# Optimization experiments

Hardware: AMD Instinct MI355X
Metric: run time of the kernel (lower is better)

Reference implementation:

```python
import jax, jax.numpy as jnp
import numpy as np
from jax import lax

I, H, L, O = 5, 64, 3, 1  # input_size, hidden_size, num_layers, output_size
B, T = 1024, 256


def setup_inputs() -> dict:
    key = jax.random.key(0)
    ks = jax.random.split(key, 1 + 4 * L + 2)
    inp = {"x": jax.random.normal(ks[0], (B, T, I), dtype=jnp.float32)}
    s = 1.0 / np.sqrt(H)  # PyTorch LSTM init scale
    kidx = 1
    for l in range(L):
        in_dim = I if l == 0 else H
        inp[f"w_ih{l}"] = jax.random.uniform(ks[kidx], (4 * H, in_dim), minval=-s, maxval=s); kidx += 1
        inp[f"w_hh{l}"] = jax.random.uniform(ks[kidx], (4 * H, H), minval=-s, maxval=s); kidx += 1
        inp[f"b_ih{l}"] = jax.random.uniform(ks[kidx], (4 * H,), minval=-s, maxval=s); kidx += 1
        inp[f"b_hh{l}"] = jax.random.uniform(ks[kidx], (4 * H,), minval=-s, maxval=s); kidx += 1
    inp["w_fc"] = jax.random.uniform(ks[kidx], (O, H), minval=-s, maxval=s); kidx += 1
    inp["b_fc"] = jax.random.uniform(ks[kidx], (O,), minval=-s, maxval=s)
    return inp


def _lstm_layer(x, w_ih, w_hh, b_ih, b_hh):
    # x: [B, T, in_dim] -> hidden sequence [B, T, H]
    b, t = x.shape[0], x.shape[1]
    h0 = jnp.zeros((b, H), dtype=x.dtype)
    c0 = jnp.zeros((b, H), dtype=x.dtype)
    # precompute input contribution for all timesteps (one big GEMM)
    xg = jnp.einsum('bti,gi->btg', x, w_ih) + (b_ih + b_hh)  # [B, T, 4H]

    def step(carry, xg_t):
        h, c = carry
        gates = xg_t + h @ w_hh.T  # [B, 4H], PyTorch gate order: i, f, g, o
        i, f, g, o = jnp.split(gates, 4, axis=-1)
        i = jax.nn.sigmoid(i)
        f = jax.nn.sigmoid(f)
        g = jnp.tanh(g)
        o = jax.nn.sigmoid(o)
        c = f * c + i * g
        h = o * jnp.tanh(c)
        return (h, c), h

    _, hs = lax.scan(step, (h0, c0), jnp.swapaxes(xg, 0, 1))  # hs: [T, B, H]
    return jnp.swapaxes(hs, 0, 1)


def reference(x, w_ih0, w_hh0, b_ih0, b_hh0, w_ih1, w_hh1, b_ih1, b_hh1,
              w_ih2, w_hh2, b_ih2, b_hh2, w_fc, b_fc):
    out = _lstm_layer(x, w_ih0, w_hh0, b_ih0, b_hh0)
    out = _lstm_layer(out, w_ih1, w_hh1, b_ih1, b_hh1)
    out = _lstm_layer(out, w_ih2, w_hh2, b_ih2, b_hh2)
    # dropout is identity in eval mode
    return out[:, -1, :] @ w_fc.T + b_fc  # [B, O]
```

## Files before the change

kernel.cpp:

```cpp
#include <hip/hip_runtime.h>
#include <math.h>


typedef __attribute__((ext_vector_type(8))) short bf16x8;
typedef __attribute__((ext_vector_type(4))) float f32x4;

constexpr int Hh  = 64;
constexpr int Tt  = 256;
constexpr int In  = 5;
constexpr int TBr = 4;
constexpr int NB  = 256;
constexpr int NT  = 768;

constexpr int RB_ = 144;
constexpr int LB  = 2304;
constexpr int PB  = 8192;

__device__ __forceinline__ float tanhc(float x) {
    return fmaf(2.0f, __builtin_amdgcn_rcpf(1.0f + __expf(-2.0f * x)), -1.0f);
}

__device__ __forceinline__ short f2bf_rne(float f) {
    union { float f; unsigned u; } v; v.f = f;
    unsigned r = (v.u + 0x7fffu + ((v.u >> 16) & 1u)) >> 16;
    return (short)r;
}
__device__ __forceinline__ void split_bf(float f, short& hi, short& lo) {
    union { float f; unsigned u; } v; v.f = f;
    hi = (short)(v.u >> 16);
    union { unsigned u; float f; } h; h.u = v.u & 0xffff0000u;
    float r = f - h.f;
    union { float f; unsigned u; } w; w.f = r;
    lo = (short)(w.u >> 16);
}

__device__ __forceinline__ bf16x8 ldwfrag(const float* __restrict__ W,
                                          int n, int stride, int k0, int kmax) {
    bf16x8 r;
    #pragma unroll
    for (int j = 0; j < 8; ++j) {
        int k = k0 + j;
        float f = (k < kmax) ? W[n * stride + k] : 0.0f;
        r[j] = f2bf_rne(f);
    }
    return r;
}

#define MF(A, B, C) __builtin_amdgcn_mfma_f32_16x16x32_bf16(A, B, C, 0, 0, 0)

#define LBAR() asm volatile("s_waitcnt lgkmcnt(0)\n\ts_barrier" ::: "memory")

#define STEP(TI, RO, RBp, WR) do {                                           \
    const int ti_ = (TI);                                                    \
    const bool act_ = (wg == 0) ? (ti_ < Tt)                                 \
                    : (wg == 1) ? (ti_ >= 1 && ti_ <= Tt)                    \
                                : (ti_ >= 2);                                \
    if (act_) {                                                              \
        if (xmask) {                   \
            _Pragma("unroll")                                                \
            for (int jj = 0; jj < In; ++jj) {                                \
                short h_, l_; split_bf(xr[jj], h_, l_);                      \
                xhi[jj] = h_; xlo[jj] = l_;                                  \
            }                                                                \
        }                                                                    \
        if (lreal) {             \
            oh0 = *(const bf16x8*)(RO);                                      \
            oh1 = *(const bf16x8*)((RO) + 64);                               \
            if (wg > 0) {                                                    \
                bh0 = *(const bf16x8*)(RBp);                                 \
                bh1 = *(const bf16x8*)((RBp) + 64);                          \
            }                                                                \
        }                                                                    \
        f32x4 acc[4];                                                        \
        __builtin_amdgcn_s_setprio(1);                                       \
        _Pragma("unroll")                                                    \
        for (int gi = 0; gi < 4; ++gi)                                       \
            acc[gi] = MF(oh0, WH[gi][0], bsv[gi]);            \
        _Pragma("unroll")                                                    \
        for (int gi = 0; gi < 4; ++gi)                                       \
            acc[gi] = MF(oh1, WH[gi][1], acc[gi]);                           \
        if (wg == 0) {                               \
            _Pragma("unroll")                                                \
            for (int gi = 0; gi < 4; ++gi)                                   \
                acc[gi] = MF(xhi, WI[gi][0], acc[gi]);                       \
            _Pragma("unroll")                                                \
            for (int gi = 0; gi < 4; ++gi)                                   \
                acc[gi] = MF(xlo, WI[gi][0], acc[gi]);                       \
        } else {                             \
            _Pragma("unroll")                                                \
            for (int gi = 0; gi < 4; ++gi)                                   \
                acc[gi] = MF(bh0, WI[gi][0], acc[gi]);                       \
            _Pragma("unroll")                                                \
            for (int gi = 0; gi < 4; ++gi)                                   \
                acc[gi] = MF(bh1, WI[gi][1], acc[gi]);                       \
        }                                                                    \
        __builtin_amdgcn_s_setprio(0);                                       \
        if (xmask && ti_ + 1 < Tt) {                    \
            _Pragma("unroll")                                                \
            for (int jj = 0; jj < In; ++jj)                                  \
                xr[jj] = x[xbase + (size_t)(ti_ + 1) * In + jj];             \
        }                                                                    \
          \
        float ei = __expf(-acc[0][0]);                                       \
        float ef = __expf(-acc[1][0]);                                       \
        float eg = __expf(-2.0f * acc[2][0]);                                \
        float eo = __expf(-acc[3][0]);                                       \
        float ig = (1.0f - eg) *                                             \
                   __builtin_amdgcn_rcpf((1.0f + ei) * (1.0f + eg));         \
        float fv = __builtin_amdgcn_rcpf(1.0f + ef);                         \
        float cn = fmaf(fv, c0, ig);                                         \
        c0 = cn;                                                             \
        float ov = __builtin_amdgcn_rcpf(1.0f + eo);                         \
        float hn = ov * tanhc(cn);                                           \
        unsigned pk_;                                                        \
        asm("v_cvt_pk_bf16_f32 %0, %1, %2" : "=v"(pk_) : "v"(hn), "v"(hn));  \
        *(short*)(WR) = (short)pk_;                                          \
        if (wg == 2) h2f[kg][ub + col] = hn;        \
    }                                                                        \
    LBAR();                                                                  \
} while (0)

__global__ __launch_bounds__(NT, 2) void lstm3_mfma(
    const float* __restrict__ x,
    const float* __restrict__ w_ih0, const float* __restrict__ w_hh0,
    const float* __restrict__ b_ih0, const float* __restrict__ b_hh0,
    const float* __restrict__ w_ih1, const float* __restrict__ w_hh1,
    const float* __restrict__ b_ih1, const float* __restrict__ b_hh1,
    const float* __restrict__ w_ih2, const float* __restrict__ w_hh2,
    const float* __restrict__ b_ih2, const float* __restrict__ b_hh2,
    const float* __restrict__ w_fc,  const float* __restrict__ b_fc,
    float* __restrict__ out)
{
    __shared__ short hb[2][PB / 2];
    __shared__ float h2f[TBr][Hh];

    const int tid = threadIdx.x;
    const int l   = tid & 63;
    const int wid = tid >> 6;
    const int wg  = wid >> 2;
    const int w4  = wid & 3;
    const int ub  = w4 * 16;
    const int col = l & 15;
    const int kg  = l >> 4;
    const int b0  = blockIdx.x * TBr;
    const bool lreal = ((col & 3) == 0);

    for (int i = tid; i < PB * 2 / 4; i += NT) ((int*)hb)[i] = 0;

    const float* whh = (wg == 0) ? w_hh0 : (wg == 1) ? w_hh1 : w_hh2;
    const float* wih = (wg == 0) ? w_ih0 : (wg == 1) ? w_ih1 : w_ih2;
    const float* bih = (wg == 0) ? b_ih0 : (wg == 1) ? b_ih1 : b_ih2;
    const float* bhh = (wg == 0) ? b_hh0 : (wg == 1) ? b_hh1 : b_hh2;

    bf16x8 WH[4][2], WI[4][2];
    f32x4  bsv[4];
    #pragma unroll
    for (int gi = 0; gi < 4; ++gi) {
        int n = gi * 64 + ub + col;
        float bs_ = bih[n] + bhh[n];
        bsv[gi] = (f32x4){bs_, bs_, bs_, bs_};
        #pragma unroll
        for (int kt = 0; kt < 2; ++kt) {
            WH[gi][kt] = ldwfrag(whh, n, Hh, kt * 32 + kg * 8, Hh);
            if (wg == 0) {
                WI[gi][kt] = (kt == 0) ? ldwfrag(wih, n, In, kg * 8, In)
                                       : ldwfrag(wih, n, In, 64, 0);
            } else {
                WI[gi][kt] = ldwfrag(wih, n, Hh, kt * 32 + kg * 8, Hh);
            }
        }
    }

    char* hbB = (char*)hb;
    const int lbelow = (wg > 0) ? (wg - 1) : 0;
    const int lown   = (wg > 0) ? LB : 0;
    const char* rbB_ = hbB + lbelow * LB + col * RB_ + kg * 16;
    const char* rbA_ = rbB_ + PB;
    const char* roA  = rbA_ + lown;
    const char* roB  = rbB_ + lown;
    char* wrA = hbB + wg * LB + (kg * 4) * RB_ + (ub + col) * 2;
    char* wrB = wrA + PB;

    const bool xmask = (wg == 0) && (kg == 0) && lreal;
    const size_t xbase = (size_t)(b0 + (col >> 2)) * Tt * In;
    float xr[5] = {0.f, 0.f, 0.f, 0.f, 0.f};
    bf16x8 xhi, xlo, oh0, oh1, bh0, bh1;
    #pragma unroll
    for (int j = 0; j < 8; ++j) {
        xhi[j] = 0; xlo[j] = 0; oh0[j] = 0; oh1[j] = 0; bh0[j] = 0; bh1[j] = 0;
    }
    if (xmask) {
        #pragma unroll
        for (int j = 0; j < In; ++j) xr[j] = x[xbase + j];
    }

    float c0 = 0.f;

    __syncthreads();

    #pragma unroll 1
    for (int t2 = 0; t2 < Tt + 2; t2 += 2) {
        STEP(t2,     roA, rbA_, wrA);
        STEP(t2 + 1, roB, rbB_, wrB);
    }

    if (tid < TBr) {
        const int b = tid;
        float accf = b_fc[0];
        #pragma unroll 1
        for (int u = 0; u < Hh; ++u)
            accf = fmaf(h2f[b][u], w_fc[u], accf);
        out[b0 + b] = accf;
    }
}

extern "C" void kernel_launch(void* const* d_in, const int* in_sizes, int n_in,
                              void* d_out, int out_size, void* d_ws, size_t ws_size,
                              hipStream_t stream) {
    const float* x     = (const float*)d_in[0];
    const float* w_ih0 = (const float*)d_in[1];
    const float* w_hh0 = (const float*)d_in[2];
    const float* b_ih0 = (const float*)d_in[3];
    const float* b_hh0 = (const float*)d_in[4];
    const float* w_ih1 = (const float*)d_in[5];
    const float* w_hh1 = (const float*)d_in[6];
    const float* b_ih1 = (const float*)d_in[7];
    const float* b_hh1 = (const float*)d_in[8];
    const float* w_ih2 = (const float*)d_in[9];
    const float* w_hh2 = (const float*)d_in[10];
    const float* b_ih2 = (const float*)d_in[11];
    const float* b_hh2 = (const float*)d_in[12];
    const float* w_fc  = (const float*)d_in[13];
    const float* b_fc  = (const float*)d_in[14];
    float* out = (float*)d_out;

    lstm3_mfma<<<NB, NT, 0, stream>>>(x,
        w_ih0, w_hh0, b_ih0, b_hh0,
        w_ih1, w_hh1, b_ih1, b_hh1,
        w_ih2, w_hh2, b_ih2, b_hh2,
        w_fc, b_fc, out);
}
```

Before: 264.4 us.

## Split LSTM step into staggered MFMA and gate phases across layers

Replaces the fused per-timestep STEP macro with a half-step loop. Each barrier interval now runs either the MFMA accumulation or the gate nonlinearity and state update, with per-layer offsets (1, 4, 7). Layers 0 and 2 run MFMA while layer 1 runs its gate math, and the reverse, so matrix-unit and transcendental/VALU work from different wave groups can overlap. The cost is roughly twice as many workgroup barriers per timestep and accumulators kept live across a barrier.

```diff
diff --git a/kernel.cpp b/kernel.cpp
--- a/kernel.cpp
+++ b/kernel.cpp
@@ -49,76 +49,6 @@
 #define MF(A, B, C) __builtin_amdgcn_mfma_f32_16x16x32_bf16(A, B, C, 0, 0, 0)
 
 #define LBAR() asm volatile("s_waitcnt lgkmcnt(0)\n\ts_barrier" ::: "memory")
-
-#define STEP(TI, RO, RBp, WR) do {                                           \
-    const int ti_ = (TI);                                                    \
-    const bool act_ = (wg == 0) ? (ti_ < Tt)                                 \
-                    : (wg == 1) ? (ti_ >= 1 && ti_ <= Tt)                    \
-                                : (ti_ >= 2);                                \
-    if (act_) {                                                              \
-        if (xmask) {                   \
-            _Pragma("unroll")                                                \
-            for (int jj = 0; jj < In; ++jj) {                                \
-                short h_, l_; split_bf(xr[jj], h_, l_);                      \
-                xhi[jj] = h_; xlo[jj] = l_;                                  \
-            }                                                                \
-        }                                                                    \
-        if (lreal) {             \
-            oh0 = *(const bf16x8*)(RO);                                      \
-            oh1 = *(const bf16x8*)((RO) + 64);                               \
-            if (wg > 0) {                                                    \
-                bh0 = *(const bf16x8*)(RBp);                                 \
-                bh1 = *(const bf16x8*)((RBp) + 64);                          \
-            }                                                                \
-        }                                                                    \
-        f32x4 acc[4];                                                        \
-        __builtin_amdgcn_s_setprio(1);                                       \
-        _Pragma("unroll")                                                    \
-        for (int gi = 0; gi < 4; ++gi)                                       \
-            acc[gi] = MF(oh0, WH[gi][0], bsv[gi]);            \
-        _Pragma("unroll")                                                    \
-        for (int gi = 0; gi < 4; ++gi)                                       \
-            acc[gi] = MF(oh1, WH[gi][1], acc[gi]);                           \
-        if (wg == 0) {                               \
-            _Pragma("unroll")                                                \
-            for (int gi = 0; gi < 4; ++gi)                                   \
-                acc[gi] = MF(xhi, WI[gi][0], acc[gi]);                       \
-            _Pragma("unroll")                                                \
-            for (int gi = 0; gi < 4; ++gi)                                   \
-                acc[gi] = MF(xlo, WI[gi][0], acc[gi]);                       \
-        } else {                             \
-            _Pragma("unroll")                                                \
-            for (int gi = 0; gi < 4; ++gi)                                   \
-                acc[gi] = MF(bh0, WI[gi][0], acc[gi]);                       \
-            _Pragma("unroll")                                                \
-            for (int gi = 0; gi < 4; ++gi)                                   \
-                acc[gi] = MF(bh1, WI[gi][1], acc[gi]);                       \
-        }                                                                    \
-        __builtin_amdgcn_s_setprio(0);                                       \
-        if (xmask && ti_ + 1 < Tt) {                    \
-            _Pragma("unroll")                                                \
-            for (int jj = 0; jj < In; ++jj)                                  \
-                xr[jj] = x[xbase + (size_t)(ti_ + 1) * In + jj];             \
-        }                                                                    \
-          \
-        float ei = __expf(-acc[0][0]);                                       \
-        float ef = __expf(-acc[1][0]);                                       \
-        float eg = __expf(-2.0f * acc[2][0]);                                \
-        float eo = __expf(-acc[3][0]);                                       \
-        float ig = (1.0f - eg) *                                             \
-                   __builtin_amdgcn_rcpf((1.0f + ei) * (1.0f + eg));         \
-        float fv = __builtin_amdgcn_rcpf(1.0f + ef);                         \
-        float cn = fmaf(fv, c0, ig);                                         \
-        c0 = cn;                                                             \
-        float ov = __builtin_amdgcn_rcpf(1.0f + eo);                         \
-        float hn = ov * tanhc(cn);                                           \
-        unsigned pk_;                                                        \
-        asm("v_cvt_pk_bf16_f32 %0, %1, %2" : "=v"(pk_) : "v"(hn), "v"(hn));  \
-        *(short*)(WR) = (short)pk_;                                          \
-        if (wg == 2) h2f[kg][ub + col] = hn;        \
-    }                                                                        \
-    LBAR();                                                                  \
-} while (0)
 
 __global__ __launch_bounds__(NT, 2) void lstm3_mfma(
     const float* __restrict__ x,
@@ -174,12 +104,12 @@
     char* hbB = (char*)hb;
     const int lbelow = (wg > 0) ? (wg - 1) : 0;
     const int lown   = (wg > 0) ? LB : 0;
-    const char* rbB_ = hbB + lbelow * LB + col * RB_ + kg * 16;
-    const char* rbA_ = rbB_ + PB;
-    const char* roA  = rbA_ + lown;
-    const char* roB  = rbB_ + lown;
-    char* wrA = hbB + wg * LB + (kg * 4) * RB_ + (ub + col) * 2;
-    char* wrB = wrA + PB;
+    const char* rbP0 = hbB + lbelow * LB + col * RB_ + kg * 16;
+    const char* rbP1 = rbP0 + PB;
+    const char* roP0 = rbP0 + lown;
+    const char* roP1 = rbP1 + lown;
+    char* wrP0 = hbB + wg * LB + (kg * 4) * RB_ + (ub + col) * 2;
+    char* wrP1 = wrP0 + PB;
 
     const bool xmask = (wg == 0) && (kg == 0) && lreal;
     const size_t xbase = (size_t)(b0 + (col >> 2)) * Tt * In;
@@ -195,13 +125,91 @@
     }
 
     float c0 = 0.f;
+    f32x4 acc[4];
+    #pragma unroll
+    for (int gi = 0; gi < 4; ++gi) acc[gi] = (f32x4){0.f, 0.f, 0.f, 0.f};
+
+    const int mo = (wg == 0) ? 1 : (wg == 1) ? 4 : 7;
 
     __syncthreads();
 
     #pragma unroll 1
-    for (int t2 = 0; t2 < Tt + 2; t2 += 2) {
-        STEP(t2,     roA, rbA_, wrA);
-        STEP(t2 + 1, roB, rbB_, wrB);
+    for (int k = 0; k < 2 * Tt + 8; ++k) {
+        const int  dm   = k - mo;
+        const bool domf = (dm >= 0) && ((dm & 1) == 0) && ((dm >> 1) < Tt);
+        const int  tm   = dm >> 1;
+        const int  dc   = dm - 1;
+        const bool docmb = (dc >= 0) && ((dc & 1) == 0) && ((dc >> 1) < Tt);
+        const int  tc   = dc >> 1;
+
+        if (domf) {
+            const char* ro = (tm & 1) ? roP0 : roP1;
+            const char* rb = (tm & 1) ? rbP1 : rbP0;
+            if (xmask) {
+                #pragma unroll
+                for (int jj = 0; jj < In; ++jj) {
+                    short h_, l_; split_bf(xr[jj], h_, l_);
+                    xhi[jj] = h_; xlo[jj] = l_;
+                }
+            }
+            if (lreal) {
+                oh0 = *(const bf16x8*)(ro);
+                oh1 = *(const bf16x8*)(ro + 64);
+                if (wg > 0) {
+                    bh0 = *(const bf16x8*)(rb);
+                    bh1 = *(const bf16x8*)(rb + 64);
+                }
+            }
+            __builtin_amdgcn_s_setprio(1);
+            #pragma unroll
+            for (int gi = 0; gi < 4; ++gi)
+                acc[gi] = MF(oh0, WH[gi][0], bsv[gi]);
+            #pragma unroll
+            for (int gi = 0; gi < 4; ++gi)
+                acc[gi] = MF(oh1, WH[gi][1], acc[gi]);
+            if (wg == 0) {
+                #pragma unroll
+                for (int gi = 0; gi < 4; ++gi)
+                    acc[gi] = MF(xhi, WI[gi][0], acc[gi]);
+                #pragma unroll
+                for (int gi = 0; gi < 4; ++gi)
+                    acc[gi] = MF(xlo, WI[gi][0], acc[gi]);
+            } else {
+                #pragma unroll
+                for (int gi = 0; gi < 4; ++gi)
+                    acc[gi] = MF(bh0, WI[gi][0], acc[gi]);
+                #pragma unroll
+                for (int gi = 0; gi < 4; ++gi)
+                    acc[gi] = MF(bh1, WI[gi][1], acc[gi]);
+            }
+            __builtin_amdgcn_s_setprio(0);
+            if (xmask && tm + 1 < Tt) {
+                #pragma unroll
+                for (int jj = 0; jj < In; ++jj)
+                    xr[jj] = x[xbase + (size_t)(tm + 1) * In + jj];
+            }
+        }
+
+        if (docmb) {
+            float ei = __expf(-acc[0][0]);
+            float ef = __expf(-acc[1][0]);
+            float eg = __expf(-2.0f * acc[2][0]);
+            float eo = __expf(-acc[3][0]);
+            float ig = (1.0f - eg) *
+                       __builtin_amdgcn_rcpf((1.0f + ei) * (1.0f + eg));
+            float fv = __builtin_amdgcn_rcpf(1.0f + ef);
+            float cn = fmaf(fv, c0, ig);
+            c0 = cn;
+            float ov = __builtin_amdgcn_rcpf(1.0f + eo);
+            float hn = ov * tanhc(cn);
+            unsigned pk_;
+            asm("v_cvt_pk_bf16_f32 %0, %1, %2" : "=v"(pk_) : "v"(hn), "v"(hn));
+            char* wr = (tc & 1) ? wrP1 : wrP0;
+            *(short*)wr = (short)pk_;
+            if (wg == 2) h2f[kg][ub + col] = hn;
+        }
+
+        LBAR();
     }
 
     if (tid < TBr) {
```

Measured after the change: 296.5 us. +12.2%, slower.

## Replace block barriers with per-wave LDS flag spin-waits and quad-buffered hidden state

Applied to the files above, without the earlier changes.

Replaces the per-timestep workgroup barrier with per-wave progress flags in shared memory. Each wave spins until the waves it depends on (same layer at t-1, layer below at t, layer above at t-3) have published. Hidden-state buffers grow from two to four so layers can drift apart without a global lockstep wavefront schedule. This is meant to remove barrier stalls and let layers run decoupled, at the cost of spin polling on LDS and a bounded spin-count escape that could silently break correctness if it triggers.

```diff
diff --git a/kernel.cpp b/kernel.cpp
--- a/kernel.cpp
+++ b/kernel.cpp
@@ -15,6 +15,7 @@
 constexpr int RB_ = 144;
 constexpr int LB  = 2304;
 constexpr int PB  = 8192;
+constexpr int NS  = 4;
 
 __device__ __forceinline__ float tanhc(float x) {
     return fmaf(2.0f, __builtin_amdgcn_rcpf(1.0f + __expf(-2.0f * x)), -1.0f);
@@ -47,60 +48,77 @@
 }
 
 #define MF(A, B, C) __builtin_amdgcn_mfma_f32_16x16x32_bf16(A, B, C, 0, 0, 0)
-
-#define LBAR() asm volatile("s_waitcnt lgkmcnt(0)\n\ts_barrier" ::: "memory")
-
-#define STEP(TI, RO, RBp, WR) do {                                           \
-    const int ti_ = (TI);                                                    \
-    const bool act_ = (wg == 0) ? (ti_ < Tt)                                 \
-                    : (wg == 1) ? (ti_ >= 1 && ti_ <= Tt)                    \
-                                : (ti_ >= 2);                                \
-    if (act_) {                                                              \
-        if (xmask) {                   \
-            _Pragma("unroll")                                                \
-            for (int jj = 0; jj < In; ++jj) {                                \
-                short h_, l_; split_bf(xr[jj], h_, l_);                      \
-                xhi[jj] = h_; xlo[jj] = l_;                                  \
+#define LKW() asm volatile("s_waitcnt lgkmcnt(0)" ::: "memory")
+
+#define STEP(T, ROFF, BOFF, WOFF) do {                                       \
+    const int t_ = (T);                                                      \
+         \
+    {                                                                        \
+        const int nO = t_ - 1;                                               \
+        int spins = 0;                                                       \
+        for (;;) {                                                           \
+            bool ok = (vfl[wg4 + 0] >= nO) & (vfl[wg4 + 1] >= nO)            \
+                    & (vfl[wg4 + 2] >= nO) & (vfl[wg4 + 3] >= nO);           \
+            if (wg > 0) {                                                    \
+                const int nB = t_;                                           \
+                ok = ok & (vfl[wg4 - 4] >= nB) & (vfl[wg4 - 3] >= nB)        \
+                        & (vfl[wg4 - 2] >= nB) & (vfl[wg4 - 1] >= nB);       \
             }                                                                \
+            if (wg < 2) {                                                    \
+                const int nA = t_ - 3;                                       \
+                ok = ok & (vfl[wg4 + 4] >= nA) & (vfl[wg4 + 5] >= nA)        \
+                        & (vfl[wg4 + 6] >= nA) & (vfl[wg4 + 7] >= nA);       \
+            }                                                                \
+            if (ok) break;                                                   \
+            if (++spins > 100000) break;        \
         }                                                                    \
-        if (lreal) {             \
-            oh0 = *(const bf16x8*)(RO);                                      \
-            oh1 = *(const bf16x8*)((RO) + 64);                               \
-            if (wg > 0) {                                                    \
-                bh0 = *(const bf16x8*)(RBp);                                 \
-                bh1 = *(const bf16x8*)((RBp) + 64);                          \
-            }                                                                \
+    }                                                                        \
+    if (xmask) {                       \
+        _Pragma("unroll")                                                    \
+        for (int jj = 0; jj < In; ++jj) {                                    \
+            short h_, l_; split_bf(xr[jj], h_, l_);                          \
+            xhi[jj] = h_; xlo[jj] = l_;                                      \
         }                                                                    \
-        f32x4 acc[4];                                                        \
-        __builtin_amdgcn_s_setprio(1);                                       \
-        _Pragma("unroll")                                                    \
-        for (int gi = 0; gi < 4; ++gi)                                       \
-            acc[gi] = MF(oh0, WH[gi][0], bsv[gi]);            \
-        _Pragma("unroll")                                                    \
-        for (int gi = 0; gi < 4; ++gi)                                       \
-            acc[gi] = MF(oh1, WH[gi][1], acc[gi]);                           \
-        if (wg == 0) {                               \
-            _Pragma("unroll")                                                \
-            for (int gi = 0; gi < 4; ++gi)                                   \
-                acc[gi] = MF(xhi, WI[gi][0], acc[gi]);                       \
-            _Pragma("unroll")                                                \
-            for (int gi = 0; gi < 4; ++gi)                                   \
-                acc[gi] = MF(xlo, WI[gi][0], acc[gi]);                       \
-        } else {                             \
-            _Pragma("unroll")                                                \
-            for (int gi = 0; gi < 4; ++gi)                                   \
-                acc[gi] = MF(bh0, WI[gi][0], acc[gi]);                       \
-            _Pragma("unroll")                                                \
-            for (int gi = 0; gi < 4; ++gi)                                   \
-                acc[gi] = MF(bh1, WI[gi][1], acc[gi]);                       \
+    }                                                                        \
+    if (lreal) {                 \
+        oh0 = *(const bf16x8*)(roB + (ROFF));                                \
+        oh1 = *(const bf16x8*)(roB + (ROFF) + 64);                           \
+        if (wg > 0) {                                                        \
+            bh0 = *(const bf16x8*)(rbB + (BOFF));                            \
+            bh1 = *(const bf16x8*)(rbB + (BOFF) + 64);                       \
         }                                                                    \
-        __builtin_amdgcn_s_setprio(0);                                       \
-        if (xmask && ti_ + 1 < Tt) {                    \
-            _Pragma("unroll")                                                \
-            for (int jj = 0; jj < In; ++jj)                                  \
-                xr[jj] = x[xbase + (size_t)(ti_ + 1) * In + jj];             \
-        }                                                                    \
+    }                                                                        \
+    f32x4 acc[4];                                                            \
+    __builtin_amdgcn_s_setprio(1);                                           \
+    _Pragma("unroll")                                                        \
+    for (int gi = 0; gi < 4; ++gi)                                           \
+        acc[gi] = MF(oh0, WH[gi][0], bsv[gi]);                \
+    _Pragma("unroll")                                                        \
+    for (int gi = 0; gi < 4; ++gi)                                           \
+        acc[gi] = MF(oh1, WH[gi][1], acc[gi]);                               \
+    if (wg == 0) {                                   \
+        _Pragma("unroll")                                                    \
+        for (int gi = 0; gi < 4; ++gi)                                       \
+            acc[gi] = MF(xhi, WI[gi][0], acc[gi]);                           \
+        _Pragma("unroll")                                                    \
+        for (int gi = 0; gi < 4; ++gi)                                       \
+            acc[gi] = MF(xlo, WI[gi][0], acc[gi]);                           \
+    } else {                                 \
+        _Pragma("unroll")                                                    \
+        for (int gi = 0; gi < 4; ++gi)                                       \
+            acc[gi] = MF(bh0, WI[gi][0], acc[gi]);                           \
+        _Pragma("unroll")                                                    \
+        for (int gi = 0; gi < 4; ++gi)                                       \
+            acc[gi] = MF(bh1, WI[gi][1], acc[gi]);                           \
+    }                                                                        \
+    __builtin_amdgcn_s_setprio(0);                                           \
+    if (xmask && t_ + 1 < Tt) {                         \
+        _Pragma("unroll")                                                    \
+        for (int jj = 0; jj < In; ++jj)                                      \
+            xr[jj] = x[xbase + (size_t)(t_ + 1) * In + jj];                  \
+    }                                                                        \
           \
+    {                                                                        \
         float ei = __expf(-acc[0][0]);                                       \
         float ef = __expf(-acc[1][0]);                                       \
         float eg = __expf(-2.0f * acc[2][0]);                                \
@@ -114,10 +132,11 @@
         float hn = ov * tanhc(cn);                                           \
         unsigned pk_;                                                        \
         asm("v_cvt_pk_bf16_f32 %0, %1, %2" : "=v"(pk_) : "v"(hn), "v"(hn));  \
-        *(short*)(WR) = (short)pk_;                                          \
+        *(short*)(wrB + (WOFF)) = (short)pk_;                                \
         if (wg == 2) h2f[kg][ub + col] = hn;        \
     }                                                                        \
-    LBAR();                                                                  \
+    LKW();                                       \
+    if (l == 0) vfl[wg4 + w4] = t_;        \
 } while (0)
 
 __global__ __launch_bounds__(NT, 2) void lstm3_mfma(
@@ -131,21 +150,26 @@
     const float* __restrict__ w_fc,  const float* __restrict__ b_fc,
     float* __restrict__ out)
 {
-    __shared__ short hb[2][PB / 2];
+    __shared__ short hb[NS][PB / 2];
     __shared__ float h2f[TBr][Hh];
+    __shared__ alignas(16) int wflag[3][4];
 
     const int tid = threadIdx.x;
     const int l   = tid & 63;
     const int wid = tid >> 6;
     const int wg  = wid >> 2;
     const int w4  = wid & 3;
+    const int wg4 = wg * 4;
     const int ub  = w4 * 16;
     const int col = l & 15;
     const int kg  = l >> 4;
     const int b0  = blockIdx.x * TBr;
     const bool lreal = ((col & 3) == 0);
 
-    for (int i = tid; i < PB * 2 / 4; i += NT) ((int*)hb)[i] = 0;
+    volatile int* vfl = (volatile int*)wflag;
+
+    for (int i = tid; i < NS * PB / 4; i += NT) ((int*)hb)[i] = 0;
+    if (tid < 12) ((int*)wflag)[tid] = -1;
 
     const float* whh = (wg == 0) ? w_hh0 : (wg == 1) ? w_hh1 : w_hh2;
     const float* wih = (wg == 0) ? w_ih0 : (wg == 1) ? w_ih1 : w_ih2;
@@ -173,13 +197,9 @@
 
     char* hbB = (char*)hb;
     const int lbelow = (wg > 0) ? (wg - 1) : 0;
-    const int lown   = (wg > 0) ? LB : 0;
-    const char* rbB_ = hbB + lbelow * LB + col * RB_ + kg * 16;
-    const char* rbA_ = rbB_ + PB;
-    const char* roA  = rbA_ + lown;
-    const char* roB  = rbB_ + lown;
-    char* wrA = hbB + wg * LB + (kg * 4) * RB_ + (ub + col) * 2;
-    char* wrB = wrA + PB;
+    const char* roB = hbB + wg     * LB + col * RB_ + kg * 16;
+    const char* rbB = hbB + lbelow * LB + col * RB_ + kg * 16;
+    char* wrB = hbB + wg * LB + (kg * 4) * RB_ + (ub + col) * 2;
 
     const bool xmask = (wg == 0) && (kg == 0) && lreal;
     const size_t xbase = (size_t)(b0 + (col >> 2)) * Tt * In;
@@ -199,10 +219,14 @@
     __syncthreads();
 
     #pragma unroll 1
-    for (int t2 = 0; t2 < Tt + 2; t2 += 2) {
-        STEP(t2,     roA, rbA_, wrA);
-        STEP(t2 + 1, roB, rbB_, wrB);
-    }
+    for (int t4 = 0; t4 < Tt; t4 += 4) {
+        STEP(t4 + 0, 3 * PB, 0,      0     );
+        STEP(t4 + 1, 0,      PB,     PB    );
+        STEP(t4 + 2, PB,     2 * PB, 2 * PB);
+        STEP(t4 + 3, 2 * PB, 3 * PB, 3 * PB);
+    }
+
+    __syncthreads();
 
     if (tid < TBr) {
         const int b = tid;
```

New measurement: 391.9 us. 48.3% more time.
